# Kernel optimization log

Hardware: AMD Instinct MI355X
Metric: run time of the kernel (lower is better)

Reference implementation:

```python
import jax, jax.numpy as jnp
import numpy as np

SCALE = 2
R_MAX = 3
ALPHA_DYN = 2.0
NEG_INF = -1e9
EPS_SIG = 1e-6

HL = WL = DL = 32
HH = WH = DH = 64
C_FEAT = 32
G_GUIDE = 3


def setup_inputs() -> dict:
    key = jax.random.key(0)
    k = jax.random.split(key, 6)
    feat_lr = jax.random.normal(k[0], (1, C_FEAT, HL, WL, DL), jnp.float32)
    guide_hr = jax.random.normal(k[1], (1, G_GUIDE, HH, WH, DH), jnp.float32)
    log_s = float(np.log(1.5))
    log_sr = float(np.log(0.1))
    sx_raw = log_s + 0.05 * jax.random.normal(k[2], (1, 1, HL, WL, DL), jnp.float32)
    sy_raw = log_s + 0.05 * jax.random.normal(k[3], (1, 1, HL, WL, DL), jnp.float32)
    sz_raw = log_s + 0.05 * jax.random.normal(k[4], (1, 1, HL, WL, DL), jnp.float32)
    sr_raw = log_sr + 0.05 * jax.random.normal(k[5], (1, 1, HL, WL, DL), jnp.float32)
    return {"feat_lr": feat_lr, "guide_hr": guide_hr, "sx_raw": sx_raw,
            "sy_raw": sy_raw, "sz_raw": sz_raw, "sr_raw": sr_raw}


def _resize3(x, shape):
    # F.interpolate(mode='trilinear', align_corners=False) == half-pixel linear resize
    return jax.image.resize(x, shape, method='trilinear')


def reference(feat_lr, guide_hr, sx_raw, sy_raw, sz_raw, sr_raw):
    C, Hl, Wl, Dl = feat_lr.shape[1:]
    G, Hh, Wh, Dh = guide_hr.shape[1:]
    feat = feat_lr[0].astype(jnp.float32)          # [C,Hl,Wl,Dl]
    guide = guide_hr[0].astype(jnp.float32)        # [G,Hh,Wh,Dh]
    # sigma maps (exp of learnable log-sigmas), clamp_min applied on maps (== on gathers)
    sx = jnp.maximum(jnp.exp(sx_raw[0, 0]), EPS_SIG)   # [Hl,Wl,Dl]
    sy = jnp.maximum(jnp.exp(sy_raw[0, 0]), EPS_SIG)
    sz = jnp.maximum(jnp.exp(sz_raw[0, 0]), EPS_SIG)
    sr = jnp.maximum(jnp.exp(sr_raw[0, 0]), EPS_SIG)

    x = jnp.arange(Hh, dtype=jnp.float32)
    y = jnp.arange(Wh, dtype=jnp.float32)
    z = jnp.arange(Dh, dtype=jnp.float32)
    X, Y, Z = jnp.meshgrid(x, y, z, indexing='ij')    # [Hh,Wh,Dh]
    u = (X + 0.5) / SCALE - 0.5
    v = (Y + 0.5) / SCALE - 0.5
    w_ = (Z + 0.5) / SCALE - 0.5
    uc = jnp.clip(jnp.round(u), 0, Hl - 1).astype(jnp.int32)
    vc = jnp.clip(jnp.round(v), 0, Wl - 1).astype(jnp.int32)
    wc = jnp.clip(jnp.round(w_), 0, Dl - 1).astype(jnp.int32)

    sigma_eff = jnp.maximum(sx, jnp.maximum(sy, sz))
    sigma_eff_hr = _resize3(sigma_eff, (Hh, Wh, Dh))
    R_map = jnp.clip(jnp.ceil(ALPHA_DYN * sigma_eff_hr), 1.0, float(R_MAX))  # [Hh,Wh,Dh]
    R2 = R_map * R_map

    guide_lr = _resize3(guide, (G, Hl, Wl, Dl))        # [G,Hl,Wl,Dl]

    offs = np.arange(-R_MAX, R_MAX + 1)
    dXg, dYg, dZg = np.meshgrid(offs, offs, offs, indexing='ij')
    offsets = jnp.asarray(np.stack([dXg.ravel(), dYg.ravel(), dZg.ravel()], 1),
                          dtype=jnp.int32)            # [343,3]

    num0 = jnp.zeros((C, Hh, Wh, Dh), jnp.float32)
    den0 = jnp.zeros((Hh, Wh, Dh), jnp.float32)
    m0 = jnp.full((Hh, Wh, Dh), NEG_INF, jnp.float32)

    def step(carry, off):
        num, den, m = carry
        dX, dY, dZ = off[0], off[1], off[2]
        Ui = jnp.clip(uc + dX, 0, Hl - 1)              # [Hh,Wh,Dh]
        Vi = jnp.clip(vc + dY, 0, Wl - 1)
        Wi = jnp.clip(wc + dZ, 0, Dl - 1)
        r2 = (dX * dX + dY * dY + dZ * dZ).astype(jnp.float32)
        mask = r2 <= R2
        cx = (Ui.astype(jnp.float32) + 0.5) * SCALE - 0.5
        cy = (Vi.astype(jnp.float32) + 0.5) * SCALE - 0.5
        cz = (Wi.astype(jnp.float32) + 0.5) * SCALE - 0.5
        dx = X - cx
        dy = Y - cy
        dz = Z - cz
        sxg = sx[Ui, Vi, Wi]
        syg = sy[Ui, Vi, Wi]
        szg = sz[Ui, Vi, Wi]
        srg = sr[Ui, Vi, Wi]
        log_ws = -dx * dx / (2 * sxg * sxg) - dy * dy / (2 * syg * syg) - dz * dz / (2 * szg * szg)
        g0 = guide_lr[:, Ui, Vi, Wi]                   # [G,Hh,Wh,Dh]
        diff2 = jnp.sum((guide - g0) ** 2, axis=0)
        log_wr = -diff2 / (2 * srg * srg + 1e-8)
        log_w = jnp.where(mask, log_ws + log_wr, NEG_INF)
        # online log-sum-exp merge (flash-attention style)
        m_new = jnp.maximum(m, log_w)
        scale_old = jnp.exp(m - m_new)
        wgt = jnp.exp(log_w - m_new)
        f = feat[:, Ui, Vi, Wi]                        # [C,Hh,Wh,Dh]
        num = num * scale_old + f * wgt
        den = den * scale_old + wgt
        return (num, den, m_new), None

    (num, den, _), _ = jax.lax.scan(step, (num0, den0, m0), offsets)
    out = (num / jnp.maximum(den, 1e-8))[None]         # [1,C,Hh,Wh,Dh]
    return out.astype(feat_lr.dtype)
```

## Files before the change

kernel.cpp:

```cpp
#include <hip/hip_runtime.h>

typedef float f32x2 __attribute__((ext_vector_type(2)));
typedef _Float16 h2 __attribute__((ext_vector_type(2)));

constexpr float LOG2E = 1.4426950408889634f;
#define TBIG 3.0e38f

struct OffTab { int v[123]; };
constexpr OffTab make_off() {
    OffTab t{}; int n = 0;
    for (int rr = 0; rr <= 9; ++rr)
        for (int a = -3; a <= 3; ++a)
            for (int b = -3; b <= 3; ++b)
                for (int c = -3; c <= 3; ++c)
                    if (a*a + b*b + c*c == rr)
                        t.v[n++] = (a + 3) | ((b + 3) << 4) | ((c + 3) << 8) | (rr << 12);
    return t;
}
__constant__ OffTab OFFT = make_off();

__device__ __forceinline__ float fast_exp2(float x) { return __builtin_amdgcn_exp2f(x); }

__device__ __forceinline__ void mk_taps(int j, int idx[4], float wt[4]) {
    float s = 0.f;
#pragma unroll
    for (int k = 0; k < 4; ++k) {
        int i = 2 * j - 1 + k;
        float w = (k == 0 || k == 3) ? 0.25f : 0.75f;
        bool ok = (i >= 0) && (i < 64);
        wt[k] = ok ? w : 0.f;
        idx[k] = ok ? i : 0;
        s += wt[k];
    }
    float inv = 1.f / s;
#pragma unroll
    for (int k = 0; k < 4; ++k) wt[k] *= inv;
}

__global__ void prepAB(const float* __restrict__ sxr, const float* __restrict__ syr,
                       const float* __restrict__ szr, const float* __restrict__ srr,
                       const float* __restrict__ guide,
                       float4* __restrict__ param4, float* __restrict__ sigEff) {
    int t = blockIdx.x * 256 + threadIdx.x;
    float sx = fmaxf(expf(sxr[t]), 1e-6f);
    float sy = fmaxf(expf(syr[t]), 1e-6f);
    float sz = fmaxf(expf(szr[t]), 1e-6f);
    float sr = fmaxf(expf(srr[t]), 1e-6f);
    param4[2 * t] = make_float4(0.5f / (sx * sx), 0.5f / (sy * sy),
                                0.5f / (sz * sz), 1.0f / (2.0f * sr * sr + 1e-8f));
    sigEff[t] = fmaxf(sx, fmaxf(sy, sz));

    int w = t & 31, v = (t >> 5) & 31, u = t >> 10;
    int iu[4], iv[4], iw[4];
    float wu[4], wv[4], ww[4];
    mk_taps(u, iu, wu);
    mk_taps(v, iv, wv);
    mk_taps(w, iw, ww);
    float g0 = 0.f, g1 = 0.f, g2 = 0.f;
#pragma unroll
    for (int a = 0; a < 4; ++a)
#pragma unroll
        for (int b = 0; b < 4; ++b) {
            float wab = wu[a] * wv[b];
            int base = iu[a] * 4096 + iv[b] * 64;
#pragma unroll
            for (int c = 0; c < 4; ++c) {
                float wt = wab * ww[c];
                int gi = base + iw[c];
                g0 += wt * guide[gi];
                g1 += wt * guide[262144 + gi];
                g2 += wt * guide[524288 + gi];
            }
        }
    param4[2 * t + 1] = make_float4(g0, g1, g2, 0.f);
}

__global__ void prepT(const float* __restrict__ feat, _Float16* __restrict__ featH) {
    __shared__ float tile[32][33];
    int uv = blockIdx.x;
    int u = uv >> 5, v = uv & 31;
    int col = threadIdx.x & 31;
    int row = threadIdx.x >> 5;
#pragma unroll
    for (int it = 0; it < 4; ++it) {
        int c = row + it * 8;
        tile[c][col] = feat[((c * 32 + u) * 32 + v) * 32 + col];
    }
    __syncthreads();
#pragma unroll
    for (int it = 0; it < 4; ++it) {
        int w = row + it * 8;
        featH[((u * 32 + v) * 32 + w) * 32 + col] = (_Float16)tile[col][w];
    }
}

__global__ __launch_bounds__(256, 4)
void jbu_main(const float* __restrict__ guide, const float4* __restrict__ param4,
              const float* __restrict__ sigEff, const _Float16* __restrict__ featH,
              float* __restrict__ out) {
    __shared__ float mbuf[2][64][33];
    __shared__ float sxch[2][2][64];
    int tid = threadIdx.x;
    int widx = tid >> 6;
    int l = tid & 63;
    int par = widx & 1;
    int q = widx >> 1;
    int bsw = (blockIdx.x & 7) * 256 + (blockIdx.x >> 3);
    int tIdx = bsw * 2 + q;
    int X = tIdx >> 6;
    int Y0 = ((tIdx >> 3) & 7) << 3;
    int Z0 = (tIdx & 7) << 3;
    int y = l >> 3, z = l & 7;
    int Y = Y0 + y, Z = Z0 + z;
    int h = ((y & 1) << 1) | (z & 1);
    int vox = (X << 12) + (Y << 6) + Z;

    float G0 = guide[vox];
    float G1 = guide[262144 + vox];
    float G2 = guide[524288 + vox];

    int x0 = max((X - 1) >> 1, 0), x1 = min(((X - 1) >> 1) + 1, 31);
    int y0 = max((Y - 1) >> 1, 0), y1 = min(((Y - 1) >> 1) + 1, 31);
    int z0 = max((Z - 1) >> 1, 0), z1 = min(((Z - 1) >> 1) + 1, 31);
    float wx1 = (X & 1) ? 0.25f : 0.75f, wx0 = 1.f - wx1;
    float wy1 = (Y & 1) ? 0.25f : 0.75f, wy0 = 1.f - wy1;
    float wz1 = (Z & 1) ? 0.25f : 0.75f, wz0 = 1.f - wz1;
#define SG(i, j, k) sigEff[((i) * 32 + (j)) * 32 + (k)]
    float se =
        wx0 * (wy0 * (wz0 * SG(x0, y0, z0) + wz1 * SG(x0, y0, z1)) +
               wy1 * (wz0 * SG(x0, y1, z0) + wz1 * SG(x0, y1, z1))) +
        wx1 * (wy0 * (wz0 * SG(x1, y0, z0) + wz1 * SG(x1, y0, z1)) +
               wy1 * (wz0 * SG(x1, y1, z0) + wz1 * SG(x1, y1, z1)));
#undef SG
    float Rf = fminf(fmaxf(ceilf(2.f * se), 1.f), 3.f);
    int R2i = (int)(Rf * Rf + 0.5f);
    bool a9 = __any((int)(R2i >= 9));
    bool a4 = __any((int)(R2i >= 4));
    int nmax = a9 ? 123 : (a4 ? 33 : 7);
    int jcount = (nmax - par + 1) >> 1;

    int ucm = (X >> 1) - 3;
    int vcm = (Y >> 1) - 3, wcm = (Z >> 1) - 3;
    float Xh = (float)X - 0.5f, Yh = (float)Y - 0.5f, Zh = (float)Z - 0.5f;

    float tmin = TBIG;
    {
        int pk_n = OFFT.v[par];
        int Ui_n = min(max(ucm + (pk_n & 15), 0), 31);
        int Vi_n = min(max(vcm + ((pk_n >> 4) & 15), 0), 31);
        int Wi_n = min(max(wcm + ((pk_n >> 8) & 15), 0), 31);
        int ci_n = (Ui_n << 10) | (Vi_n << 5) | Wi_n;
        float4 A_n = param4[2 * ci_n];
        float4 B_n = param4[2 * ci_n + 1];
#pragma unroll 2
        for (int j = 0; j < jcount; ++j) {
            int pk = pk_n, Ui = Ui_n, Vi = Vi_n, Wi = Wi_n;
            float4 A = A_n, B = B_n;
            int on = min(2 * j + 2 + par, nmax - 1);
            pk_n = OFFT.v[on];
            Ui_n = min(max(ucm + (pk_n & 15), 0), 31);
            Vi_n = min(max(vcm + ((pk_n >> 4) & 15), 0), 31);
            Wi_n = min(max(wcm + ((pk_n >> 8) & 15), 0), 31);
            ci_n = (Ui_n << 10) | (Vi_n << 5) | Wi_n;
            A_n = param4[2 * ci_n];
            B_n = param4[2 * ci_n + 1];

            int r2 = pk >> 12;
            float ddx = fmaf(-2.f, (float)Ui, Xh);
            float ddy = fmaf(-2.f, (float)Vi, Yh);
            float ddz = fmaf(-2.f, (float)Wi, Zh);
            float tt = fmaf(ddx * ddx, A.x, fmaf(ddy * ddy, A.y, ddz * ddz * A.z));
            float d0 = G0 - B.x, d1 = G1 - B.y, d2 = G2 - B.z;
            tt = fmaf(fmaf(d0, d0, fmaf(d1, d1, d2 * d2)), A.w, tt);
            tmin = fminf(tmin, (r2 <= R2i) ? tt : TBIG);
        }
    }
    sxch[q][par][l] = tmin;
    __syncthreads();
    tmin = fminf(tmin, sxch[q][par ^ 1][l]);
    float ML = tmin * LOG2E;

    f32x2 num2[4][4];
#pragma unroll
    for (int r = 0; r < 4; ++r)
#pragma unroll
        for (int p = 0; p < 4; ++p) num2[r][p] = {0.f, 0.f};
    float den = 0.f;
    {
        int pk_n = OFFT.v[par];
        int Ui_n = min(max(ucm + (pk_n & 15), 0), 31);
        int Vi_n = min(max(vcm + ((pk_n >> 4) & 15), 0), 31);
        int Wi_n = min(max(wcm + ((pk_n >> 8) & 15), 0), 31);
        int ci_n = (Ui_n << 10) | (Vi_n << 5) | Wi_n;
        float4 A_n = param4[2 * ci_n];
        float4 B_n = param4[2 * ci_n + 1];
        float4 F_n = *(const float4*)(featH + ci_n * 32 + h * 8);
#pragma unroll 2
        for (int j = 0; j < jcount; ++j) {
            int pk = pk_n, Ui = Ui_n, Vi = Vi_n, Wi = Wi_n;
            float4 A = A_n, B = B_n, F = F_n;
            int on = min(2 * j + 2 + par, nmax - 1);
            pk_n = OFFT.v[on];
            Ui_n = min(max(ucm + (pk_n & 15), 0), 31);
            Vi_n = min(max(vcm + ((pk_n >> 4) & 15), 0), 31);
            Wi_n = min(max(wcm + ((pk_n >> 8) & 15), 0), 31);
            ci_n = (Ui_n << 10) | (Vi_n << 5) | Wi_n;
            A_n = param4[2 * ci_n];
            B_n = param4[2 * ci_n + 1];
            F_n = *(const float4*)(featH + ci_n * 32 + h * 8);

            int r2 = pk >> 12;
            float ddx = fmaf(-2.f, (float)Ui, Xh);
            float ddy = fmaf(-2.f, (float)Vi, Yh);
            float ddz = fmaf(-2.f, (float)Wi, Zh);
            float tt = fmaf(ddx * ddx, A.x, fmaf(ddy * ddy, A.y, ddz * ddz * A.z));
            float d0 = G0 - B.x, d1 = G1 - B.y, d2 = G2 - B.z;
            tt = fmaf(fmaf(d0, d0, fmaf(d1, d1, d2 * d2)), A.w, tt);
            tt = (r2 <= R2i) ? tt : TBIG;
            float wgt = fast_exp2(fmaf(tt, -LOG2E, ML));
            den += wgt;
            float w1 = __shfl_xor(wgt, 1), w8 = __shfl_xor(wgt, 8), w9 = __shfl_xor(wgt, 9);

            h2 q0 = __builtin_bit_cast(h2, F.x);
            h2 q1 = __builtin_bit_cast(h2, F.y);
            h2 q2 = __builtin_bit_cast(h2, F.z);
            h2 q3 = __builtin_bit_cast(h2, F.w);
            f32x2 f0 = {(float)q0.x, (float)q0.y};
            f32x2 f1 = {(float)q1.x, (float)q1.y};
            f32x2 f2 = {(float)q2.x, (float)q2.y};
            f32x2 f3 = {(float)q3.x, (float)q3.y};
            f32x2 w0v = {wgt, wgt}, w1v = {w1, w1}, w2v = {w8, w8}, w3v = {w9, w9};
            num2[0][0] += f0 * w0v; num2[0][1] += f1 * w0v; num2[0][2] += f2 * w0v; num2[0][3] += f3 * w0v;
            num2[1][0] += f0 * w1v; num2[1][1] += f1 * w1v; num2[1][2] += f2 * w1v; num2[1][3] += f3 * w1v;
            num2[2][0] += f0 * w2v; num2[2][1] += f1 * w2v; num2[2][2] += f2 * w2v; num2[2][3] += f3 * w2v;
            num2[3][0] += f0 * w3v; num2[3][1] += f1 * w3v; num2[3][2] += f2 * w3v; num2[3][3] += f3 * w3v;
        }
    }

    float* mp = &mbuf[q][l][0];
    if (par) {
#pragma unroll
        for (int r = 0; r < 4; ++r)
#pragma unroll
            for (int p = 0; p < 4; ++p) {
                mp[r * 8 + 2 * p] = num2[r][p].x;
                mp[r * 8 + 2 * p + 1] = num2[r][p].y;
            }
        mp[32] = den;
    }
    __syncthreads();
    if (par) return;

#pragma unroll
    for (int r = 0; r < 4; ++r)
#pragma unroll
        for (int p = 0; p < 4; ++p) {
            num2[r][p].x += mp[r * 8 + 2 * p];
            num2[r][p].y += mp[r * 8 + 2 * p + 1];
        }
    den += mp[32];

    float invd = 1.0f / fmaxf(den, 1e-8f);
    float i1 = __shfl_xor(invd, 1), i8 = __shfl_xor(invd, 8), i9 = __shfl_xor(invd, 9);
    float* ob = out + (size_t)(h * 8) * 262144;
#pragma unroll
    for (int p = 0; p < 4; ++p) {
        f32x2 v0 = num2[0][p], v1 = num2[1][p], v2 = num2[2][p], v3 = num2[3][p];
        ob[(2 * p) * 262144 + vox] = v0.x * invd;
        ob[(2 * p + 1) * 262144 + vox] = v0.y * invd;
        ob[(2 * p) * 262144 + (vox ^ 1)] = v1.x * i1;
        ob[(2 * p + 1) * 262144 + (vox ^ 1)] = v1.y * i1;
        ob[(2 * p) * 262144 + (vox ^ 64)] = v2.x * i8;
        ob[(2 * p + 1) * 262144 + (vox ^ 64)] = v2.y * i8;
        ob[(2 * p) * 262144 + (vox ^ 65)] = v3.x * i9;
        ob[(2 * p + 1) * 262144 + (vox ^ 65)] = v3.y * i9;
    }
}

extern "C" void kernel_launch(void* const* d_in, const int* in_sizes, int n_in,
                              void* d_out, int out_size, void* d_ws, size_t ws_size,
                              hipStream_t stream) {
    const float* feat = (const float*)d_in[0];
    const float* guide = (const float*)d_in[1];
    const float* sxr = (const float*)d_in[2];
    const float* syr = (const float*)d_in[3];
    const float* szr = (const float*)d_in[4];
    const float* srr = (const float*)d_in[5];
    float* out = (float*)d_out;

    char* ws = (char*)d_ws;
    float4* param4 = (float4*)ws;
    float* sigEff = (float*)(ws + 1048576);
    _Float16* featH = (_Float16*)(ws + 1179648);

    prepAB<<<128, 256, 0, stream>>>(sxr, syr, szr, srr, guide, param4, sigEff);
    prepT<<<1024, 256, 0, stream>>>(feat, featH);
    jbu_main<<<2048, 256, 0, stream>>>(guide, param4, sigEff, featH, out);
}
```

Baseline: 119.6 us.

## Replace two-pass max with chunked online softmax and padded border-free neighbor tables

```diff
diff --git a/kernel.cpp b/kernel.cpp
--- a/kernel.cpp
+++ b/kernel.cpp
@@ -5,19 +5,36 @@
 
 constexpr float LOG2E = 1.4426950408889634f;
 #define TBIG 3.0e38f
-
-struct OffTab { int v[123]; };
-constexpr OffTab make_off() {
-    OffTab t{}; int n = 0;
+#define PD 38
+#define PD2 1444
+#define NPC 54872
+
+struct Tabs { int ti[2][62][4]; float tf[2][62][4]; };
+constexpr Tabs make_tabs() {
+    int dxs[123], dys[123], dzs[123]; int n = 0;
     for (int rr = 0; rr <= 9; ++rr)
         for (int a = -3; a <= 3; ++a)
             for (int b = -3; b <= 3; ++b)
                 for (int c = -3; c <= 3; ++c)
-                    if (a*a + b*b + c*c == rr)
-                        t.v[n++] = (a + 3) | ((b + 3) << 4) | ((c + 3) << 8) | (rr << 12);
-    return t;
-}
-__constant__ OffTab OFFT = make_off();
+                    if (a*a + b*b + c*c == rr) { dxs[n]=a; dys[n]=b; dzs[n]=c; ++n; }
+    Tabs T{};
+    for (int p = 0; p < 2; ++p)
+        for (int j = 0; j < 62; ++j) {
+            int k = 2*j + p;
+            if (k < 123) {
+                int a = dxs[k], b = dys[k], c = dzs[k];
+                int tci = (a*PD + b)*PD + c;
+                T.ti[p][j][0] = tci*32;
+                T.ti[p][j][1] = a*a + b*b + c*c;
+                T.ti[p][j][2] = (a+3) | ((b+3)<<8) | ((c+3)<<16);
+                T.tf[p][j][0] = 2.f*a; T.tf[p][j][1] = 2.f*b; T.tf[p][j][2] = 2.f*c;
+            } else {
+                T.ti[p][j][0] = 0; T.ti[p][j][1] = 999; T.ti[p][j][2] = 3 | (3<<8) | (3<<16);
+            }
+        }
+    return T;
+}
+__constant__ Tabs TB = make_tabs();
 
 __device__ __forceinline__ float fast_exp2(float x) { return __builtin_amdgcn_exp2f(x); }
 
@@ -25,7 +42,7 @@
     float s = 0.f;
 #pragma unroll
     for (int k = 0; k < 4; ++k) {
-        int i = 2 * j - 1 + k;
+        int i = 2*j - 1 + k;
         float w = (k == 0 || k == 3) ? 0.25f : 0.75f;
         bool ok = (i >= 0) && (i < 64);
         wt[k] = ok ? w : 0.f;
@@ -37,45 +54,45 @@
     for (int k = 0; k < 4; ++k) wt[k] *= inv;
 }
 
-__global__ void prepAB(const float* __restrict__ sxr, const float* __restrict__ syr,
-                       const float* __restrict__ szr, const float* __restrict__ srr,
-                       const float* __restrict__ guide,
-                       float4* __restrict__ param4, float* __restrict__ sigEff) {
+__global__ void prepABpad(const float* __restrict__ sxr, const float* __restrict__ syr,
+                          const float* __restrict__ szr, const float* __restrict__ srr,
+                          const float* __restrict__ guide,
+                          float4* __restrict__ param4, float* __restrict__ sigEff) {
     int t = blockIdx.x * 256 + threadIdx.x;
-    float sx = fmaxf(expf(sxr[t]), 1e-6f);
-    float sy = fmaxf(expf(syr[t]), 1e-6f);
-    float sz = fmaxf(expf(szr[t]), 1e-6f);
-    float sr = fmaxf(expf(srr[t]), 1e-6f);
-    param4[2 * t] = make_float4(0.5f / (sx * sx), 0.5f / (sy * sy),
-                                0.5f / (sz * sz), 1.0f / (2.0f * sr * sr + 1e-8f));
-    sigEff[t] = fmaxf(sx, fmaxf(sy, sz));
-
-    int w = t & 31, v = (t >> 5) & 31, u = t >> 10;
+    if (t >= NPC) return;
+    int pu = t / PD2; int rem = t - pu*PD2; int pv = rem / PD; int pw = rem - pv*PD;
+    int u = min(max(pu-3, 0), 31), v = min(max(pv-3, 0), 31), w = min(max(pw-3, 0), 31);
+    int ci = (u*32 + v)*32 + w;
+    float sx = fmaxf(expf(sxr[ci]), 1e-6f);
+    float sy = fmaxf(expf(syr[ci]), 1e-6f);
+    float sz = fmaxf(expf(szr[ci]), 1e-6f);
+    float sr = fmaxf(expf(srr[ci]), 1e-6f);
+    param4[2*t] = make_float4(0.5f/(sx*sx), 0.5f/(sy*sy), 0.5f/(sz*sz), 1.0f/(2.0f*sr*sr + 1e-8f));
+    if (pu-3 == u && pv-3 == v && pw-3 == w) sigEff[ci] = fmaxf(sx, fmaxf(sy, sz));
+
     int iu[4], iv[4], iw[4];
     float wu[4], wv[4], ww[4];
-    mk_taps(u, iu, wu);
-    mk_taps(v, iv, wv);
-    mk_taps(w, iw, ww);
+    mk_taps(u, iu, wu); mk_taps(v, iv, wv); mk_taps(w, iw, ww);
     float g0 = 0.f, g1 = 0.f, g2 = 0.f;
 #pragma unroll
     for (int a = 0; a < 4; ++a)
 #pragma unroll
         for (int b = 0; b < 4; ++b) {
-            float wab = wu[a] * wv[b];
-            int base = iu[a] * 4096 + iv[b] * 64;
+            float wab = wu[a]*wv[b];
+            int base = iu[a]*4096 + iv[b]*64;
 #pragma unroll
             for (int c = 0; c < 4; ++c) {
-                float wt = wab * ww[c];
+                float wt = wab*ww[c];
                 int gi = base + iw[c];
-                g0 += wt * guide[gi];
-                g1 += wt * guide[262144 + gi];
-                g2 += wt * guide[524288 + gi];
+                g0 += wt*guide[gi];
+                g1 += wt*guide[262144 + gi];
+                g2 += wt*guide[524288 + gi];
             }
         }
-    param4[2 * t + 1] = make_float4(g0, g1, g2, 0.f);
-}
-
-__global__ void prepT(const float* __restrict__ feat, _Float16* __restrict__ featH) {
+    param4[2*t + 1] = make_float4(g0, g1, g2, 0.f);
+}
+
+__global__ void prepTpad(const float* __restrict__ feat, _Float16* __restrict__ featH) {
     __shared__ float tile[32][33];
     int uv = blockIdx.x;
     int u = uv >> 5, v = uv & 31;
@@ -83,14 +100,108 @@
     int row = threadIdx.x >> 5;
 #pragma unroll
     for (int it = 0; it < 4; ++it) {
-        int c = row + it * 8;
-        tile[c][col] = feat[((c * 32 + u) * 32 + v) * 32 + col];
+        int c = row + it*8;
+        tile[c][col] = feat[((c*32 + u)*32 + v)*32 + col];
     }
     __syncthreads();
 #pragma unroll
     for (int it = 0; it < 4; ++it) {
-        int w = row + it * 8;
-        featH[((u * 32 + v) * 32 + w) * 32 + col] = (_Float16)tile[col][w];
+        int w = row + it*8;
+        int pci = (u+3)*PD2 + (v+3)*PD + (w+3);
+        featH[pci*32 + col] = (_Float16)tile[col][w];
+    }
+}
+
+__global__ void prepBorder(_Float16* __restrict__ featH) {
+    int t = blockIdx.x * 256 + threadIdx.x;
+    if (t >= NPC) return;
+    int pu = t / PD2; int rem = t - pu*PD2; int pv = rem / PD; int pw = rem - pv*PD;
+    int u = min(max(pu-3, 0), 31), v = min(max(pv-3, 0), 31), w = min(max(pw-3, 0), 31);
+    if (pu-3 == u && pv-3 == v && pw-3 == w) return;
+    int src = ((u+3)*PD2 + (v+3)*PD + (w+3))*32;
+    uint4* d = (uint4*)(featH + t*32);
+    const uint4* s = (const uint4*)(featH + src);
+    d[0] = s[0]; d[1] = s[1]; d[2] = s[2]; d[3] = s[3];
+}
+
+template<bool INTER>
+__device__ __forceinline__ void body(const float4* __restrict__ param4,
+                                     const _Float16* __restrict__ featH,
+                                     int par, int pbase, int fbase, int jcount, int R2i,
+                                     int uc, int vc, int wc,
+                                     float exf, float eyf, float ezf,
+                                     float Xh, float Yh, float Zh,
+                                     float G0, float G1, float G2,
+                                     f32x2 (&num2)[4][4], float& den, float& M) {
+    for (int c = 0; c < 2; ++c) {
+        float tts[31];
+        float cmin = TBIG;
+#pragma unroll
+        for (int j = 0; j < 31; ++j) {
+            int jg = c*31 + j;
+            int e0  = TB.ti[par][jg][0];
+            int er2 = TB.ti[par][jg][1];
+            const char* pA = (const char*)param4 + (pbase + e0);
+            float4 A  = *(const float4*)pA;
+            float4 Bv = *(const float4*)(pA + 16);
+            float ddx, ddy, ddz;
+            if (INTER) {
+                ddx = exf - TB.tf[par][jg][0];
+                ddy = eyf - TB.tf[par][jg][1];
+                ddz = ezf - TB.tf[par][jg][2];
+            } else {
+                int epk = TB.ti[par][jg][2];
+                int Ui = min(max(uc + ((epk & 255) - 3), 0), 31);
+                int Vi = min(max(vc + (((epk >> 8) & 255) - 3), 0), 31);
+                int Wi = min(max(wc + ((epk >> 16) - 3), 0), 31);
+                ddx = fmaf(-2.f, (float)Ui, Xh);
+                ddy = fmaf(-2.f, (float)Vi, Yh);
+                ddz = fmaf(-2.f, (float)Wi, Zh);
+            }
+            float tt = fmaf(ddx*ddx, A.x, fmaf(ddy*ddy, A.y, ddz*ddz*A.z));
+            float d0 = G0 - Bv.x, d1 = G1 - Bv.y, d2 = G2 - Bv.z;
+            tt = fmaf(fmaf(d0, d0, fmaf(d1, d1, d2*d2)), A.w, tt);
+            int r2e = (jg < jcount) ? er2 : 999;
+            tt = (r2e <= R2i) ? tt : TBIG;
+            tts[j] = tt;
+            cmin = fminf(cmin, tt);
+        }
+        float Mn = fminf(M, cmin);
+        float f = fast_exp2((Mn - M) * LOG2E);
+        M = Mn;
+        float f1 = __shfl_xor(f, 1), f8 = __shfl_xor(f, 8), f9 = __shfl_xor(f, 9);
+        den *= f;
+        f32x2 fv0 = {f, f}, fv1 = {f1, f1}, fv2 = {f8, f8}, fv3 = {f9, f9};
+#pragma unroll
+        for (int p = 0; p < 4; ++p) {
+            num2[0][p] *= fv0;
+            num2[1][p] *= fv1;
+            num2[2][p] *= fv2;
+            num2[3][p] *= fv3;
+        }
+        float MLc = M * LOG2E;
+#pragma unroll
+        for (int j = 0; j < 31; ++j) {
+            int jg = c*31 + j;
+            int e0 = TB.ti[par][jg][0];
+            float wgt = fast_exp2(fmaf(tts[j], -LOG2E, MLc));
+            den += wgt;
+            float w1 = __shfl_xor(wgt, 1), w8 = __shfl_xor(wgt, 8), w9 = __shfl_xor(wgt, 9);
+            float4 F = *(const float4*)(featH + (fbase + e0));
+            h2 q0 = __builtin_bit_cast(h2, F.x);
+            h2 q1 = __builtin_bit_cast(h2, F.y);
+            h2 q2 = __builtin_bit_cast(h2, F.z);
+            h2 q3 = __builtin_bit_cast(h2, F.w);
+            f32x2 f0 = {(float)q0.x, (float)q0.y};
+            f32x2 f1v = {(float)q1.x, (float)q1.y};
+            f32x2 f2v = {(float)q2.x, (float)q2.y};
+            f32x2 f3v = {(float)q3.x, (float)q3.y};
+            f32x2 w0v = {wgt, wgt}, w1v = {w1, w1}, w2v = {w8, w8}, w3v = {w9, w9};
+            num2[0][0] += f0*w0v;  num2[0][1] += f1v*w0v; num2[0][2] += f2v*w0v; num2[0][3] += f3v*w0v;
+            num2[1][0] += f0*w1v;  num2[1][1] += f1v*w1v; num2[1][2] += f2v*w1v; num2[1][3] += f3v*w1v;
+            num2[2][0] += f0*w2v;  num2[2][1] += f1v*w2v; num2[2][2] += f2v*w2v; num2[2][3] += f3v*w2v;
+            num2[3][0] += f0*w3v;  num2[3][1] += f1v*w3v; num2[3][2] += f2v*w3v; num2[3][3] += f3v*w3v;
+        }
     }
 }
 
@@ -98,8 +209,7 @@
 void jbu_main(const float* __restrict__ guide, const float4* __restrict__ param4,
               const float* __restrict__ sigEff, const _Float16* __restrict__ featH,
               float* __restrict__ out) {
-    __shared__ float mbuf[2][64][33];
-    __shared__ float sxch[2][2][64];
+    __shared__ float mbuf[2][64][34];
     int tid = threadIdx.x;
     int widx = tid >> 6;
     int l = tid & 63;
@@ -119,123 +229,52 @@
     float G1 = guide[262144 + vox];
     float G2 = guide[524288 + vox];
 
-    int x0 = max((X - 1) >> 1, 0), x1 = min(((X - 1) >> 1) + 1, 31);
-    int y0 = max((Y - 1) >> 1, 0), y1 = min(((Y - 1) >> 1) + 1, 31);
-    int z0 = max((Z - 1) >> 1, 0), z1 = min(((Z - 1) >> 1) + 1, 31);
+    int x0 = max((X-1) >> 1, 0), x1 = min(((X-1) >> 1) + 1, 31);
+    int y0 = max((Y-1) >> 1, 0), y1 = min(((Y-1) >> 1) + 1, 31);
+    int z0 = max((Z-1) >> 1, 0), z1 = min(((Z-1) >> 1) + 1, 31);
     float wx1 = (X & 1) ? 0.25f : 0.75f, wx0 = 1.f - wx1;
     float wy1 = (Y & 1) ? 0.25f : 0.75f, wy0 = 1.f - wy1;
     float wz1 = (Z & 1) ? 0.25f : 0.75f, wz0 = 1.f - wz1;
-#define SG(i, j, k) sigEff[((i) * 32 + (j)) * 32 + (k)]
+#define SG(i, j, k) sigEff[((i)*32 + (j))*32 + (k)]
     float se =
-        wx0 * (wy0 * (wz0 * SG(x0, y0, z0) + wz1 * SG(x0, y0, z1)) +
-               wy1 * (wz0 * SG(x0, y1, z0) + wz1 * SG(x0, y1, z1))) +
-        wx1 * (wy0 * (wz0 * SG(x1, y0, z0) + wz1 * SG(x1, y0, z1)) +
-               wy1 * (wz0 * SG(x1, y1, z0) + wz1 * SG(x1, y1, z1)));
+        wx0*(wy0*(wz0*SG(x0,y0,z0) + wz1*SG(x0,y0,z1)) +
+             wy1*(wz0*SG(x0,y1,z0) + wz1*SG(x0,y1,z1))) +
+        wx1*(wy0*(wz0*SG(x1,y0,z0) + wz1*SG(x1,y0,z1)) +
+             wy1*(wz0*SG(x1,y1,z0) + wz1*SG(x1,y1,z1)));
 #undef SG
-    float Rf = fminf(fmaxf(ceilf(2.f * se), 1.f), 3.f);
-    int R2i = (int)(Rf * Rf + 0.5f);
+    float Rf = fminf(fmaxf(ceilf(2.f*se), 1.f), 3.f);
+    int R2i = (int)(Rf*Rf + 0.5f);
     bool a9 = __any((int)(R2i >= 9));
     bool a4 = __any((int)(R2i >= 4));
     int nmax = a9 ? 123 : (a4 ? 33 : 7);
     int jcount = (nmax - par + 1) >> 1;
 
-    int ucm = (X >> 1) - 3;
-    int vcm = (Y >> 1) - 3, wcm = (Z >> 1) - 3;
+    int uc = X >> 1, vc = Y >> 1, wc = Z >> 1;
     float Xh = (float)X - 0.5f, Yh = (float)Y - 0.5f, Zh = (float)Z - 0.5f;
-
-    float tmin = TBIG;
-    {
-        int pk_n = OFFT.v[par];
-        int Ui_n = min(max(ucm + (pk_n & 15), 0), 31);
-        int Vi_n = min(max(vcm + ((pk_n >> 4) & 15), 0), 31);
-        int Wi_n = min(max(wcm + ((pk_n >> 8) & 15), 0), 31);
-        int ci_n = (Ui_n << 10) | (Vi_n << 5) | Wi_n;
-        float4 A_n = param4[2 * ci_n];
-        float4 B_n = param4[2 * ci_n + 1];
-#pragma unroll 2
-        for (int j = 0; j < jcount; ++j) {
-            int pk = pk_n, Ui = Ui_n, Vi = Vi_n, Wi = Wi_n;
-            float4 A = A_n, B = B_n;
-            int on = min(2 * j + 2 + par, nmax - 1);
-            pk_n = OFFT.v[on];
-            Ui_n = min(max(ucm + (pk_n & 15), 0), 31);
-            Vi_n = min(max(vcm + ((pk_n >> 4) & 15), 0), 31);
-            Wi_n = min(max(wcm + ((pk_n >> 8) & 15), 0), 31);
-            ci_n = (Ui_n << 10) | (Vi_n << 5) | Wi_n;
-            A_n = param4[2 * ci_n];
-            B_n = param4[2 * ci_n + 1];
-
-            int r2 = pk >> 12;
-            float ddx = fmaf(-2.f, (float)Ui, Xh);
-            float ddy = fmaf(-2.f, (float)Vi, Yh);
-            float ddz = fmaf(-2.f, (float)Wi, Zh);
-            float tt = fmaf(ddx * ddx, A.x, fmaf(ddy * ddy, A.y, ddz * ddz * A.z));
-            float d0 = G0 - B.x, d1 = G1 - B.y, d2 = G2 - B.z;
-            tt = fmaf(fmaf(d0, d0, fmaf(d1, d1, d2 * d2)), A.w, tt);
-            tmin = fminf(tmin, (r2 <= R2i) ? tt : TBIG);
-        }
-    }
-    sxch[q][par][l] = tmin;
-    __syncthreads();
-    tmin = fminf(tmin, sxch[q][par ^ 1][l]);
-    float ML = tmin * LOG2E;
+    float exf = (float)(X - 2*uc) - 0.5f;
+    float eyf = (float)(Y - 2*vc) - 0.5f;
+    float ezf = (float)(Z - 2*wc) - 0.5f;
+
+    int pci = (uc+3)*PD2 + (vc+3)*PD + (wc+3);
+    int pbase = pci*32;
+    int fbase = pci*32 + h*8;
+
+    int vc0 = Y0 >> 1, wc0 = Z0 >> 1;
+    bool inter = (uc >= 3 && uc <= 28 && vc0 >= 3 && vc0 <= 25 && wc0 >= 3 && wc0 <= 25);
 
     f32x2 num2[4][4];
 #pragma unroll
     for (int r = 0; r < 4; ++r)
 #pragma unroll
         for (int p = 0; p < 4; ++p) num2[r][p] = {0.f, 0.f};
-    float den = 0.f;
-    {
-        int pk_n = OFFT.v[par];
-        int Ui_n = min(max(ucm + (pk_n & 15), 0), 31);
-        int Vi_n = min(max(vcm + ((pk_n >> 4) & 15), 0), 31);
-        int Wi_n = min(max(wcm + ((pk_n >> 8) & 15), 0), 31);
-        int ci_n = (Ui_n << 10) | (Vi_n << 5) | Wi_n;
-        float4 A_n = param4[2 * ci_n];
-        float4 B_n = param4[2 * ci_n + 1];
-        float4 F_n = *(const float4*)(featH + ci_n * 32 + h * 8);
-#pragma unroll 2
-        for (int j = 0; j < jcount; ++j) {
-            int pk = pk_n, Ui = Ui_n, Vi = Vi_n, Wi = Wi_n;
-            float4 A = A_n, B = B_n, F = F_n;
-            int on = min(2 * j + 2 + par, nmax - 1);
-            pk_n = OFFT.v[on];
-            Ui_n = min(max(ucm + (pk_n & 15), 0), 31);
-            Vi_n = min(max(vcm + ((pk_n >> 4) & 15), 0), 31);
-            Wi_n = min(max(wcm + ((pk_n >> 8) & 15), 0), 31);
-            ci_n = (Ui_n << 10) | (Vi_n << 5) | Wi_n;
-            A_n = param4[2 * ci_n];
-            B_n = param4[2 * ci_n + 1];
-            F_n = *(const float4*)(featH + ci_n * 32 + h * 8);
-
-            int r2 = pk >> 12;
-            float ddx = fmaf(-2.f, (float)Ui, Xh);
-            float ddy = fmaf(-2.f, (float)Vi, Yh);
-            float ddz = fmaf(-2.f, (float)Wi, Zh);
-            float tt = fmaf(ddx * ddx, A.x, fmaf(ddy * ddy, A.y, ddz * ddz * A.z));
-            float d0 = G0 - B.x, d1 = G1 - B.y, d2 = G2 - B.z;
-            tt = fmaf(fmaf(d0, d0, fmaf(d1, d1, d2 * d2)), A.w, tt);
-            tt = (r2 <= R2i) ? tt : TBIG;
-            float wgt = fast_exp2(fmaf(tt, -LOG2E, ML));
-            den += wgt;
-            float w1 = __shfl_xor(wgt, 1), w8 = __shfl_xor(wgt, 8), w9 = __shfl_xor(wgt, 9);
-
-            h2 q0 = __builtin_bit_cast(h2, F.x);
-            h2 q1 = __builtin_bit_cast(h2, F.y);
-            h2 q2 = __builtin_bit_cast(h2, F.z);
-            h2 q3 = __builtin_bit_cast(h2, F.w);
-            f32x2 f0 = {(float)q0.x, (float)q0.y};
-            f32x2 f1 = {(float)q1.x, (float)q1.y};
-            f32x2 f2 = {(float)q2.x, (float)q2.y};
-            f32x2 f3 = {(float)q3.x, (float)q3.y};
-            f32x2 w0v = {wgt, wgt}, w1v = {w1, w1}, w2v = {w8, w8}, w3v = {w9, w9};
-            num2[0][0] += f0 * w0v; num2[0][1] += f1 * w0v; num2[0][2] += f2 * w0v; num2[0][3] += f3 * w0v;
-            num2[1][0] += f0 * w1v; num2[1][1] += f1 * w1v; num2[1][2] += f2 * w1v; num2[1][3] += f3 * w1v;
-            num2[2][0] += f0 * w2v; num2[2][1] += f1 * w2v; num2[2][2] += f2 * w2v; num2[2][3] += f3 * w2v;
-            num2[3][0] += f0 * w3v; num2[3][1] += f1 * w3v; num2[3][2] += f2 * w3v; num2[3][3] += f3 * w3v;
-        }
-    }
+    float den = 0.f, M = TBIG;
+
+    if (inter)
+        body<true>(param4, featH, par, pbase, fbase, jcount, R2i, uc, vc, wc,
+                   exf, eyf, ezf, Xh, Yh, Zh, G0, G1, G2, num2, den, M);
+    else
+        body<false>(param4, featH, par, pbase, fbase, jcount, R2i, uc, vc, wc,
+                    exf, eyf, ezf, Xh, Yh, Zh, G0, G1, G2, num2, den, M);
 
     float* mp = &mbuf[q][l][0];
     if (par) {
@@ -243,44 +282,54 @@
         for (int r = 0; r < 4; ++r)
 #pragma unroll
             for (int p = 0; p < 4; ++p) {
-                mp[r * 8 + 2 * p] = num2[r][p].x;
-                mp[r * 8 + 2 * p + 1] = num2[r][p].y;
+                mp[r*8 + 2*p]     = num2[r][p].x;
+                mp[r*8 + 2*p + 1] = num2[r][p].y;
             }
         mp[32] = den;
+        mp[33] = M;
     }
     __syncthreads();
     if (par) return;
 
+    float denoth = mp[32], Moth = mp[33];
+    float Mc = fminf(M, Moth);
+    float fs = fast_exp2((Mc - M) * LOG2E);
+    float fo = fast_exp2((Mc - Moth) * LOG2E);
+    den = den*fs + denoth*fo;
+    float fs1 = __shfl_xor(fs, 1), fo1 = __shfl_xor(fo, 1);
+    float fs8 = __shfl_xor(fs, 8), fo8 = __shfl_xor(fo, 8);
+    float fs9 = __shfl_xor(fs, 9), fo9 = __shfl_xor(fo, 9);
+    f32x2 fsv[4] = {{fs,fs},{fs1,fs1},{fs8,fs8},{fs9,fs9}};
+    f32x2 fov[4] = {{fo,fo},{fo1,fo1},{fo8,fo8},{fo9,fo9}};
 #pragma unroll
     for (int r = 0; r < 4; ++r)
 #pragma unroll
         for (int p = 0; p < 4; ++p) {
-            num2[r][p].x += mp[r * 8 + 2 * p];
-            num2[r][p].y += mp[r * 8 + 2 * p + 1];
-        }
-    den += mp[32];
+            f32x2 o = {mp[r*8 + 2*p], mp[r*8 + 2*p + 1]};
+            num2[r][p] = num2[r][p]*fsv[r] + o*fov[r];
+        }
 
     float invd = 1.0f / fmaxf(den, 1e-8f);
     float i1 = __shfl_xor(invd, 1), i8 = __shfl_xor(invd, 8), i9 = __shfl_xor(invd, 9);
-    float* ob = out + (size_t)(h * 8) * 262144;
+    float* ob = out + (size_t)(h*8) * 262144;
 #pragma unroll
     for (int p = 0; p < 4; ++p) {
         f32x2 v0 = num2[0][p], v1 = num2[1][p], v2 = num2[2][p], v3 = num2[3][p];
-        ob[(2 * p) * 262144 + vox] = v0.x * invd;
-        ob[(2 * p + 1) * 262144 + vox] = v0.y * invd;
-        ob[(2 * p) * 262144 + (vox ^ 1)] = v1.x * i1;
-        ob[(2 * p + 1) * 262144 + (vox ^ 1)] = v1.y * i1;
-        ob[(2 * p) * 262144 + (vox ^ 64)] = v2.x * i8;
-        ob[(2 * p + 1) * 262144 + (vox ^ 64)] = v2.y * i8;
-        ob[(2 * p) * 262144 + (vox ^ 65)] = v3.x * i9;
-        ob[(2 * p + 1) * 262144 + (vox ^ 65)] = v3.y * i9;
+        ob[(2*p)*262144 + vox]          = v0.x * invd;
+        ob[(2*p+1)*262144 + vox]        = v0.y * invd;
+        ob[(2*p)*262144 + (vox ^ 1)]    = v1.x * i1;
+        ob[(2*p+1)*262144 + (vox ^ 1)]  = v1.y * i1;
+        ob[(2*p)*262144 + (vox ^ 64)]   = v2.x * i8;
+        ob[(2*p+1)*262144 + (vox ^ 64)] = v2.y * i8;
+        ob[(2*p)*262144 + (vox ^ 65)]   = v3.x * i9;
+        ob[(2*p+1)*262144 + (vox ^ 65)] = v3.y * i9;
     }
 }
 
 extern "C" void kernel_launch(void* const* d_in, const int* in_sizes, int n_in,
                               void* d_out, int out_size, void* d_ws, size_t ws_size,
                               hipStream_t stream) {
-    const float* feat = (const float*)d_in[0];
+    const float* feat  = (const float*)d_in[0];
     const float* guide = (const float*)d_in[1];
     const float* sxr = (const float*)d_in[2];
     const float* syr = (const float*)d_in[3];
@@ -289,11 +338,12 @@
     float* out = (float*)d_out;
 
     char* ws = (char*)d_ws;
-    float4* param4 = (float4*)ws;
-    float* sigEff = (float*)(ws + 1048576);
-    _Float16* featH = (_Float16*)(ws + 1179648);
-
-    prepAB<<<128, 256, 0, stream>>>(sxr, syr, szr, srr, guide, param4, sigEff);
-    prepT<<<1024, 256, 0, stream>>>(feat, featH);
+    float4* param4  = (float4*)ws;
+    float* sigEff   = (float*)(ws + 2097152);
+    _Float16* featH = (_Float16*)(ws + 2228224);
+
+    prepABpad<<<215, 256, 0, stream>>>(sxr, syr, szr, srr, guide, param4, sigEff);
+    prepTpad<<<1024, 256, 0, stream>>>(feat, featH);
+    prepBorder<<<215, 256, 0, stream>>>(featH);
     jbu_main<<<2048, 256, 0, stream>>>(guide, param4, sigEff, featH, out);
 }
```

Measured after the change: 146.3 us. 1.22x slower.
